# Kernel optimization log

Measured on AMD Instinct MI355X. Metric: run time of the kernel, lower is better.

## Reference

```python
import jax, jax.numpy as jnp
import numpy as np

H = W = 32
C = 512
RED = 16


def make_gus(v=1.5):
    # gus[p=(i,k), x, y] = exp(-((x-i)^2+(y-k)^2)/(2 v^2)) / (2 pi v^2), normalized per p.
    idx = np.arange(H, dtype=np.float64)
    d2 = (idx[:, None] - idx[None, :]) ** 2          # [center, coord]
    g1 = np.exp(-d2 / (2.0 * v * v))                  # separable factor
    g = np.einsum('ix,ky->ikxy', g1, g1) / (2.0 * np.pi * v * v)
    g = g / g.sum(axis=(2, 3), keepdims=True)         # per-position normalization
    return jnp.asarray(g.reshape(H * W, H, W), dtype=jnp.float32)


def setup_inputs() -> dict:
    key = jax.random.key(0)
    ks = jax.random.split(key, 6)
    b = 16
    return {
        'x': jax.random.normal(ks[0], (b, C, H, W), dtype=jnp.float32),
        'se_w1': jax.random.normal(ks[1], (C // RED, C), dtype=jnp.float32) * 0.02,
        'se_b1': jnp.zeros((C // RED,), dtype=jnp.float32),
        'se_w2': jax.random.normal(ks[2], (C, C // RED), dtype=jnp.float32) * 0.02,
        'se_b2': jnp.zeros((C,), dtype=jnp.float32),
        'down_w': jax.random.normal(ks[3], (C, 2 * C), dtype=jnp.float32) * 0.02,
        'gus': make_gus(1.5),
    }


def _patches3(img, h, w):
    # img: [b, c, h+2, w+2] -> [b, c, h, w, 9] (3x3 neighborhoods, row-major dy*3+dx)
    ps = [img[:, :, dy:dy + h, dx:dx + w] for dy in range(3) for dx in range(3)]
    return jnp.stack(ps, axis=-1)


def reference(x, se_w1, se_b1, se_w2, se_b2, down_w, gus):
    b, c, h, w = x.shape
    # --- SELayer ---
    s = x.mean(axis=(2, 3))                                   # [b, c]
    y = jax.nn.relu(s @ se_w1.T + se_b1)                       # [b, c/16]
    y = jax.nn.sigmoid(y @ se_w2.T + se_b2)                    # [b, c]
    out32 = x * y[:, :, None, None]
    # --- gaussian-weighted global pooling per output position ---
    # g[b, p, ch] = sum_{y,x} gus[p,y,x] * out32[b,ch,y,x]; then torch's view(c,h,w)
    gus_out = jnp.einsum('pyx,bcyx->bpc', gus, out32).reshape(b, c, h, w)
    # --- patch self-attention ---
    sig = jax.nn.sigmoid(out32)
    sigp = _patches3(jnp.pad(sig, ((0, 0), (0, 0), (1, 1), (1, 1))), h, w)    # [b,c,h,w,9]
    ffp = _patches3(jnp.pad(out32, ((0, 0), (0, 0), (1, 1), (1, 1))), h, w)   # [b,c,h,w,9]
    logits = jnp.einsum('bcyx,bcyxk->byxk', sig, sigp) / c     # mean over channels
    attn = jax.nn.softmax(logits, axis=-1)                     # softmax over 3x3 patch
    g2 = jnp.einsum('byxk,bcyxk->byxc', attn, ffp)             # [b,h,w,c] = [b, p, c]
    out_csa = g2.reshape(b, c, h, w)                           # torch view(c,h,w) of [hw,c]
    # --- down: 1x1 conv (no bias) + InstanceNorm2d + LeakyReLU(0.2) ---
    cat = jnp.concatenate([gus_out, out_csa], axis=1)          # [b, 2c, h, w]
    z = jnp.einsum('oi,biyx->boyx', down_w, cat)
    mu = z.mean(axis=(2, 3), keepdims=True)
    var = z.var(axis=(2, 3), keepdims=True)
    zn = (z - mu) * jax.lax.rsqrt(var + 1e-5)
    return jnp.where(zn >= 0, zn, 0.2 * zn)
```

## Files before the change

kernel.cpp:

```cpp
#include <hip/hip_runtime.h>
#include <stdint.h>

#define NB 16
#define NC 512
#define NS 1024
#define NR 32

typedef unsigned short u16;
typedef unsigned int u32;

typedef __attribute__((ext_vector_type(8))) short short8;
typedef __attribute__((ext_vector_type(4))) float f32x4;

__device__ __forceinline__ float bf2f(u16 u) {
    union { u32 i; float f; } c; c.i = ((u32)u) << 16; return c.f;
}
__device__ __forceinline__ u16 f2bf(float f) {
    union { float f; u32 i; } c; c.f = f;
    u32 r = (c.i + 0x7FFFu + ((c.i >> 16) & 1u)) >> 16;
    return (u16)r;
}
__device__ __forceinline__ float sigm(float x) {
    return 1.0f / (1.0f + __expf(-x));
}

__global__ void k_mean(const float* __restrict__ x, float* __restrict__ sm) {
    const int row = blockIdx.x;
    const float4* xr = (const float4*)(x + (long)row * NS);
    const int t = threadIdx.x;
    float4 v = xr[t];
    float p = v.x + v.y + v.z + v.w;
    for (int off = 32; off; off >>= 1) p += __shfl_down(p, off);
    __shared__ float red[4];
    if ((t & 63) == 0) red[t >> 6] = p;
    __syncthreads();
    if (t == 0) sm[row] = (red[0] + red[1] + red[2] + red[3]) * (1.0f / 1024.0f);
}

__global__ void k_se(const float* __restrict__ sm, const float* __restrict__ w1,
                     const float* __restrict__ b1, const float* __restrict__ w2,
                     const float* __restrict__ b2, float* __restrict__ y) {
    const int b = blockIdx.x;
    __shared__ float s_s[NC];
    __shared__ float s_y1[NR];
    const int t = threadIdx.x;
    s_s[t] = sm[b * NC + t];
    s_s[t + 256] = sm[b * NC + t + 256];
    __syncthreads();
    if (t < NR) {
        float acc = b1[t];
        for (int c = 0; c < NC; ++c) acc += s_s[c] * w1[t * NC + c];
        s_y1[t] = fmaxf(acc, 0.0f);
    }
    __syncthreads();
    for (int i = 0; i < 2; ++i) {
        int c = t + i * 256;
        float acc = b2[c];
#pragma unroll
        for (int r = 0; r < NR; ++r) acc += s_y1[r] * w2[c * NR + r];
        y[b * NC + c] = 1.0f / (1.0f + expf(-acc));
    }
}

__global__ void k_scale(const float* __restrict__ x, const float* __restrict__ y,
                        u16* __restrict__ o32, u16* __restrict__ o32t,
                        u16* __restrict__ sig_t) {
    const int b = blockIdx.z;
    const int c0 = blockIdx.y * 32;
    const int s0 = blockIdx.x * 32;
    const int tx = threadIdx.x & 31, ty = threadIdx.x >> 5;
    __shared__ float tile[32][33];
    const float* xb = x + (long)b * NC * NS;
#pragma unroll
    for (int it = 0; it < 4; ++it) {
        int c = c0 + ty + it * 8;
        float v = xb[(long)c * NS + s0 + tx] * y[b * NC + c];
        tile[ty + it * 8][tx] = v;
        o32[((long)b * NC + c) * NS + s0 + tx] = f2bf(v);
    }
    __syncthreads();
#pragma unroll
    for (int it = 0; it < 4; ++it) {
        int sr = ty + it * 8;
        float tv = tile[tx][sr];
        long idx = ((long)b * NS + (s0 + sr)) * NC + c0 + tx;
        o32t[idx] = f2bf(tv);
        sig_t[idx] = f2bf(sigm(tv));
    }
}

__global__ void k_cvt(const float* __restrict__ g, const float* __restrict__ dw,
                      u16* __restrict__ gb, u16* __restrict__ dwb) {
    const int i = blockIdx.x * 256 + threadIdx.x;
    gb[i] = f2bf(g[i]);
    if (i < 524288) dwb[i] = f2bf(dw[i]);
}

__device__ __forceinline__ void st_out(float* p, float v) { *p = v; }
__device__ __forceinline__ void st_out(u16* p, float v) { *p = f2bf(v); }

template <typename OT>
__global__ __launch_bounds__(256, 4)
void gemm_bt(const u16* __restrict__ A, const u16* __restrict__ Bt, OT* __restrict__ Co,
             int M, int N, int K, long batA, long batB, long batC) {
    const int b = blockIdx.z;
    const u16* Ab = A + (long)b * batA;
    const u16* Bb = Bt + (long)b * batB;
    OT* Cb = Co + (long)b * batC;
    const int m0 = blockIdx.y * 128, n0 = blockIdx.x * 64;
    __shared__ __align__(16) u16 As[128 * 64];
    __shared__ __align__(16) u16 Bs[64 * 64];
    const int tid = threadIdx.x;
    const int lane = tid & 63, wave = tid >> 6;
    const int wm = (wave >> 1) * 64, wn = (wave & 1) * 32;
    f32x4 acc[4][2];
#pragma unroll
    for (int i = 0; i < 4; ++i)
#pragma unroll
        for (int j = 0; j < 2; ++j) acc[i][j] = (f32x4){0.f, 0.f, 0.f, 0.f};

    const int erow = (tid * 8) >> 6;
    const int ecol = (tid * 8) & 63;

    for (int k0 = 0; k0 < K; k0 += 64) {
#pragma unroll
        for (int q = 0; q < 4; ++q) {
            const u16* ga = Ab + (long)(m0 + q * 32 + erow) * K + (k0 + ecol);
            __builtin_amdgcn_global_load_lds(
                (const __attribute__((address_space(1))) u32*)ga,
                (__attribute__((address_space(3))) u32*)&As[q * 2048 + tid * 8], 16, 0, 0);
        }
#pragma unroll
        for (int q = 0; q < 2; ++q) {
            const u16* gb = Bb + (long)(n0 + q * 32 + erow) * K + (k0 + ecol);
            __builtin_amdgcn_global_load_lds(
                (const __attribute__((address_space(1))) u32*)gb,
                (__attribute__((address_space(3))) u32*)&Bs[q * 2048 + tid * 8], 16, 0, 0);
        }
        __syncthreads();
#pragma unroll
        for (int kk = 0; kk < 64; kk += 32) {
            const int kidx = kk + ((lane >> 4) << 3);
            short8 af[4], bfr[2];
#pragma unroll
            for (int i = 0; i < 4; ++i)
                af[i] = *(const short8*)&As[(wm + i * 16 + (lane & 15)) * 64 + kidx];
#pragma unroll
            for (int j = 0; j < 2; ++j)
                bfr[j] = *(const short8*)&Bs[(wn + j * 16 + (lane & 15)) * 64 + kidx];
#pragma unroll
            for (int i = 0; i < 4; ++i)
#pragma unroll
                for (int j = 0; j < 2; ++j)
                    acc[i][j] = __builtin_amdgcn_mfma_f32_16x16x32_bf16(af[i], bfr[j], acc[i][j], 0, 0, 0);
        }
        __syncthreads();
    }
    const int col = lane & 15, rq = (lane >> 4) * 4;
#pragma unroll
    for (int i = 0; i < 4; ++i)
#pragma unroll
        for (int j = 0; j < 2; ++j)
#pragma unroll
            for (int r = 0; r < 4; ++r) {
                int row = m0 + wm + i * 16 + rq + r;
                int ncol = n0 + wn + j * 16 + col;
                st_out(&Cb[(long)row * N + ncol], acc[i][j][r]);
            }
}

__global__ __launch_bounds__(256)
void k_attn(const u16* __restrict__ sig_t, const u16* __restrict__ o32t,
            u16* __restrict__ g2) {
    const int wave = threadIdx.x >> 6, lane = threadIdx.x & 63;
    const int tid = threadIdx.x;
    const int bx = blockIdx.x;
    const int b = blockIdx.y;
    const int y0 = bx >> 3;
    const int xbase = (bx & 7) * 4;
    const long base = (long)b * NS * NC;
    __shared__ __align__(16) u16 smem[2 * 18 * NC];

#pragma unroll
    for (int r = 0; r < 9; ++r) {
        int idx = r * 256 + tid;
        int pair = idx >> 7;
        int rem = idx & 127;
        int arr = rem >> 6;
        int ch0 = (rem & 63) * 8;
        int yy = y0 + pair / 6 - 1;
        int xx = xbase + pair % 6 - 1;
        short8 v;
        if (yy >= 0 && yy < 32 && xx >= 0 && xx < 32) {
            long roff = base + (long)(yy * 32 + xx) * NC + ch0;
            v = arr ? *(const short8*)&o32t[roff] : *(const short8*)&sig_t[roff];
        } else {
            v = (short8){0, 0, 0, 0, 0, 0, 0, 0};
        }
        *(short8*)&smem[(arr * 18 + pair) * NC + ch0] = v;
    }
    __syncthreads();

    const int coff = lane * 8;
    short8 csv = *(const short8*)&smem[(6 + wave + 1) * NC + coff];
    float sc[8];
#pragma unroll
    for (int j = 0; j < 8; ++j) sc[j] = bf2f((u16)csv[j]);

    float part[9];
#pragma unroll
    for (int k = 0; k < 9; ++k) {
        int pair = (k / 3) * 6 + wave + k % 3;
        short8 sv = *(const short8*)&smem[pair * NC + coff];
        float p = 0.f;
#pragma unroll
        for (int j = 0; j < 8; ++j) p += sc[j] * bf2f((u16)sv[j]);
        part[k] = p;
    }
#pragma unroll
    for (int k = 0; k < 9; ++k)
        for (int off = 32; off; off >>= 1) part[k] += __shfl_down(part[k], off);

    if (lane == 0) {
        float mx = -1e30f;
#pragma unroll
        for (int k = 0; k < 9; ++k) { part[k] *= (1.0f / 512.0f); mx = fmaxf(mx, part[k]); }
        float sum = 0.f;
#pragma unroll
        for (int k = 0; k < 9; ++k) { part[k] = __expf(part[k] - mx); sum += part[k]; }
        float inv = 1.0f / sum;
#pragma unroll
        for (int k = 0; k < 9; ++k) part[k] *= inv;
    }
    float g[8] = {0.f, 0.f, 0.f, 0.f, 0.f, 0.f, 0.f, 0.f};
#pragma unroll
    for (int k = 0; k < 9; ++k) {
        float a = __shfl(part[k], 0);
        int pair = (k / 3) * 6 + wave + k % 3;
        short8 rv = *(const short8*)&smem[(18 + pair) * NC + coff];
#pragma unroll
        for (int j = 0; j < 8; ++j) g[j] += a * bf2f((u16)rv[j]);
    }
    short8 ov;
#pragma unroll
    for (int j = 0; j < 8; ++j) ov[j] = (short)f2bf(g[j]);
    const int s = y0 * 32 + xbase + wave;
    *(short8*)&g2[base + (long)s * NC + coff] = ov;
}

__global__ void k_tr(const u16* __restrict__ g, const u16* __restrict__ g2,
                     u16* __restrict__ ct) {
    const int b = blockIdx.z;
    const int i0 = blockIdx.y * 32, s0 = blockIdx.x * 32;
    const int tx = threadIdx.x & 31, ty = threadIdx.x >> 5;
    __shared__ u16 tile[32][33];
    const u16* src = (i0 < 512) ? (g + (long)b * 524288 + (long)i0 * 1024)
                                : (g2 + (long)b * 524288 + (long)(i0 - 512) * 1024);
#pragma unroll
    for (int it = 0; it < 4; ++it) {
        int il = ty + it * 8;
        tile[il][tx] = src[(long)il * 1024 + s0 + tx];
    }
    __syncthreads();
#pragma unroll
    for (int it = 0; it < 4; ++it) {
        int sl = ty + it * 8;
        ct[(long)b * 1048576 + (long)(s0 + sl) * 1024 + i0 + tx] = tile[tx][sl];
    }
}

__global__ void k_norm(const float* __restrict__ z, float* __restrict__ out) {
    const int row = blockIdx.x;
    const float4* zr = (const float4*)(z + (long)row * NS);
    const int t = threadIdx.x;
    float4 v = zr[t];
    float sm = v.x + v.y + v.z + v.w;
    float sq = v.x * v.x + v.y * v.y + v.z * v.z + v.w * v.w;
    for (int off = 32; off; off >>= 1) { sm += __shfl_down(sm, off); sq += __shfl_down(sq, off); }
    __shared__ float rs[4], rq2[4];
    if ((t & 63) == 0) { rs[t >> 6] = sm; rq2[t >> 6] = sq; }
    __syncthreads();
    float tot = rs[0] + rs[1] + rs[2] + rs[3];
    float totq = rq2[0] + rq2[1] + rq2[2] + rq2[3];
    float mu = tot * (1.0f / 1024.0f);
    float var = totq * (1.0f / 1024.0f) - mu * mu;
    float sc = rsqrtf(var + 1e-5f);
    float4 o;
    float a;
    a = (v.x - mu) * sc; o.x = (a >= 0.f) ? a : 0.2f * a;
    a = (v.y - mu) * sc; o.y = (a >= 0.f) ? a : 0.2f * a;
    a = (v.z - mu) * sc; o.z = (a >= 0.f) ? a : 0.2f * a;
    a = (v.w - mu) * sc; o.w = (a >= 0.f) ? a : 0.2f * a;
    ((float4*)(out + (long)row * NS))[t] = o;
}

extern "C" void kernel_launch(void* const* d_in, const int* in_sizes, int n_in,
                              void* d_out, int out_size, void* d_ws, size_t ws_size,
                              hipStream_t stream) {
    const float* x   = (const float*)d_in[0];
    const float* w1  = (const float*)d_in[1];
    const float* b1  = (const float*)d_in[2];
    const float* w2  = (const float*)d_in[3];
    const float* b2  = (const float*)d_in[4];
    const float* dw  = (const float*)d_in[5];
    const float* gus = (const float*)d_in[6];
    float* out = (float*)d_out;
    char* ws = (char*)d_ws;

    float* sm_buf = (float*)(ws + 0);
    float* y_buf  = (float*)(ws + 32768);
    u16* gusbf    = (u16*)(ws + 65536);
    u16* dwbf     = (u16*)(ws + 2162688);
    char* regA    = ws + 3211264;
    u16* o32      = (u16*)regA;
    u16* o32t     = (u16*)(regA + 16777216);
    u16* catT     = (u16*)regA;
    char* regB    = ws + 36765696;
    u16* sig_t    = (u16*)regB;
    u16* gbuf     = (u16*)regB;
    u16* g2b      = (u16*)(regB + 16777216);
    float* Z      = (float*)regB;

    k_mean<<<dim3(NB * NC), dim3(256), 0, stream>>>(x, sm_buf);
    k_se<<<dim3(NB), dim3(256), 0, stream>>>(sm_buf, w1, b1, w2, b2, y_buf);
    k_scale<<<dim3(32, 16, NB), dim3(256), 0, stream>>>(x, y_buf, o32, o32t, sig_t);
    k_cvt<<<dim3(4096), dim3(256), 0, stream>>>(gus, dw, gusbf, dwbf);
    k_attn<<<dim3(256, NB), dim3(256), 0, stream>>>(sig_t, o32t, g2b);
    gemm_bt<u16><<<dim3(8, 8, NB), dim3(256), 0, stream>>>(
        gusbf, o32, gbuf, 1024, 512, 1024, 0L, (long)NC * NS, (long)NC * NS);
    k_tr<<<dim3(32, 32, NB), dim3(256), 0, stream>>>(gbuf, g2b, catT);
    gemm_bt<float><<<dim3(16, 4, NB), dim3(256), 0, stream>>>(
        dwbf, catT, Z, 512, 1024, 1024, 0L, (long)NS * 1024, (long)NC * NS);
    k_norm<<<dim3(NB * NC), dim3(256), 0, stream>>>(Z, out);
}
```

Before: 231.9 us.

## Merge first GEMM with attention kernel, fuse mean with convert, use 128x128 GEMM tiles

Folds the bf16 conversion of gus and down_w into the channel-mean kernel as extra blocks. Runs the gaussian-pooling GEMM and the patch-attention kernel as one launch, with block index selecting the role and dynamic shared memory shared between them, so the two independent stages can overlap. Because the GEMM output can no longer alias sig_t, which attention is still reading, it moves to a separate workspace region. The shared GEMM body switches to 128x128 tiles with a 4x4 MFMA accumulator per wave. This raises register pressure, and the new buffer needs more workspace.

```diff
diff --git a/kernel.cpp b/kernel.cpp
--- a/kernel.cpp
+++ b/kernel.cpp
@@ -24,17 +24,25 @@
     return 1.0f / (1.0f + __expf(-x));
 }
 
-__global__ void k_mean(const float* __restrict__ x, float* __restrict__ sm) {
-    const int row = blockIdx.x;
-    const float4* xr = (const float4*)(x + (long)row * NS);
+__global__ void k_mean_cvt(const float* __restrict__ x, float* __restrict__ sm,
+                           const float* __restrict__ g, const float* __restrict__ dw,
+                           u16* __restrict__ gb, u16* __restrict__ dwb) {
     const int t = threadIdx.x;
-    float4 v = xr[t];
-    float p = v.x + v.y + v.z + v.w;
-    for (int off = 32; off; off >>= 1) p += __shfl_down(p, off);
-    __shared__ float red[4];
-    if ((t & 63) == 0) red[t >> 6] = p;
-    __syncthreads();
-    if (t == 0) sm[row] = (red[0] + red[1] + red[2] + red[3]) * (1.0f / 1024.0f);
+    if (blockIdx.x < NB * NC) {
+        const int row = blockIdx.x;
+        const float4* xr = (const float4*)(x + (long)row * NS);
+        float4 v = xr[t];
+        float p = v.x + v.y + v.z + v.w;
+        for (int off = 32; off; off >>= 1) p += __shfl_down(p, off);
+        __shared__ float red[4];
+        if ((t & 63) == 0) red[t >> 6] = p;
+        __syncthreads();
+        if (t == 0) sm[row] = (red[0] + red[1] + red[2] + red[3]) * (1.0f / 1024.0f);
+    } else {
+        const int i = (blockIdx.x - NB * NC) * 256 + t;
+        gb[i] = f2bf(g[i]);
+        if (i < 524288) dwb[i] = f2bf(dw[i]);
+    }
 }
 
 __global__ void k_se(const float* __restrict__ sm, const float* __restrict__ w1,
@@ -89,69 +97,58 @@
     }
 }
 
-__global__ void k_cvt(const float* __restrict__ g, const float* __restrict__ dw,
-                      u16* __restrict__ gb, u16* __restrict__ dwb) {
-    const int i = blockIdx.x * 256 + threadIdx.x;
-    gb[i] = f2bf(g[i]);
-    if (i < 524288) dwb[i] = f2bf(dw[i]);
-}
-
 __device__ __forceinline__ void st_out(float* p, float v) { *p = v; }
 __device__ __forceinline__ void st_out(u16* p, float v) { *p = f2bf(v); }
 
 template <typename OT>
-__global__ __launch_bounds__(256, 4)
-void gemm_bt(const u16* __restrict__ A, const u16* __restrict__ Bt, OT* __restrict__ Co,
-             int M, int N, int K, long batA, long batB, long batC) {
-    const int b = blockIdx.z;
-    const u16* Ab = A + (long)b * batA;
-    const u16* Bb = Bt + (long)b * batB;
-    OT* Cb = Co + (long)b * batC;
-    const int m0 = blockIdx.y * 128, n0 = blockIdx.x * 64;
-    __shared__ __align__(16) u16 As[128 * 64];
-    __shared__ __align__(16) u16 Bs[64 * 64];
+__device__ __forceinline__
+void gemm_body(const u16* __restrict__ Ab, const u16* __restrict__ Bb,
+               OT* __restrict__ Cb, int m0, int n0, int N, int K,
+               u16* As, u16* Bs) {
     const int tid = threadIdx.x;
     const int lane = tid & 63, wave = tid >> 6;
-    const int wm = (wave >> 1) * 64, wn = (wave & 1) * 32;
-    f32x4 acc[4][2];
+    const int wm = (wave >> 1) * 64, wn = (wave & 1) * 64;
+    f32x4 acc[4][4];
 #pragma unroll
     for (int i = 0; i < 4; ++i)
 #pragma unroll
-        for (int j = 0; j < 2; ++j) acc[i][j] = (f32x4){0.f, 0.f, 0.f, 0.f};
-
-    const int erow = (tid * 8) >> 6;
-    const int ecol = (tid * 8) & 63;
+        for (int j = 0; j < 4; ++j) acc[i][j] = (f32x4){0.f, 0.f, 0.f, 0.f};
+
+    int mrow[4], kcol[4];
+#pragma unroll
+    for (int q = 0; q < 4; ++q) {
+        int eoff = wave * 2048 + q * 512 + lane * 8;
+        mrow[q] = eoff >> 6;
+        kcol[q] = eoff & 63;
+    }
 
     for (int k0 = 0; k0 < K; k0 += 64) {
 #pragma unroll
         for (int q = 0; q < 4; ++q) {
-            const u16* ga = Ab + (long)(m0 + q * 32 + erow) * K + (k0 + ecol);
+            const u16* ga = Ab + (long)(m0 + mrow[q]) * K + (k0 + kcol[q]);
             __builtin_amdgcn_global_load_lds(
                 (const __attribute__((address_space(1))) u32*)ga,
-                (__attribute__((address_space(3))) u32*)&As[q * 2048 + tid * 8], 16, 0, 0);
-        }
-#pragma unroll
-        for (int q = 0; q < 2; ++q) {
-            const u16* gb = Bb + (long)(n0 + q * 32 + erow) * K + (k0 + ecol);
+                (__attribute__((address_space(3))) u32*)&As[wave * 2048 + q * 512], 16, 0, 0);
+            const u16* gb = Bb + (long)(n0 + mrow[q]) * K + (k0 + kcol[q]);
             __builtin_amdgcn_global_load_lds(
                 (const __attribute__((address_space(1))) u32*)gb,
-                (__attribute__((address_space(3))) u32*)&Bs[q * 2048 + tid * 8], 16, 0, 0);
+                (__attribute__((address_space(3))) u32*)&Bs[wave * 2048 + q * 512], 16, 0, 0);
         }
         __syncthreads();
 #pragma unroll
         for (int kk = 0; kk < 64; kk += 32) {
             const int kidx = kk + ((lane >> 4) << 3);
-            short8 af[4], bfr[2];
+            short8 af[4], bfr[4];
 #pragma unroll
             for (int i = 0; i < 4; ++i)
                 af[i] = *(const short8*)&As[(wm + i * 16 + (lane & 15)) * 64 + kidx];
 #pragma unroll
-            for (int j = 0; j < 2; ++j)
+            for (int j = 0; j < 4; ++j)
                 bfr[j] = *(const short8*)&Bs[(wn + j * 16 + (lane & 15)) * 64 + kidx];
 #pragma unroll
             for (int i = 0; i < 4; ++i)
 #pragma unroll
-                for (int j = 0; j < 2; ++j)
+                for (int j = 0; j < 4; ++j)
                     acc[i][j] = __builtin_amdgcn_mfma_f32_16x16x32_bf16(af[i], bfr[j], acc[i][j], 0, 0, 0);
         }
         __syncthreads();
@@ -160,7 +157,7 @@
 #pragma unroll
     for (int i = 0; i < 4; ++i)
 #pragma unroll
-        for (int j = 0; j < 2; ++j)
+        for (int j = 0; j < 4; ++j)
 #pragma unroll
             for (int r = 0; r < 4; ++r) {
                 int row = m0 + wm + i * 16 + rq + r;
@@ -170,16 +167,30 @@
 }
 
 __global__ __launch_bounds__(256)
-void k_attn(const u16* __restrict__ sig_t, const u16* __restrict__ o32t,
-            u16* __restrict__ g2) {
+void k_gemm1_attn(const u16* __restrict__ gusbf, const u16* __restrict__ o32,
+                  u16* __restrict__ gbuf, const u16* __restrict__ sig_t,
+                  const u16* __restrict__ o32t, u16* __restrict__ g2) {
+    extern __shared__ __align__(16) char dsm[];
+    if (blockIdx.x < 512) {
+        const int gx = blockIdx.x;
+        const int b = gx >> 5;
+        const int m0 = ((gx >> 2) & 7) * 128;
+        const int n0 = (gx & 3) * 128;
+        u16* As = (u16*)dsm;
+        u16* Bs = As + 128 * 64;
+        gemm_body<u16>(gusbf, o32 + (long)b * NC * NS, gbuf + (long)b * NC * NS,
+                       m0, n0, 512, 1024, As, Bs);
+        return;
+    }
+    const int id = blockIdx.x - 512;
+    const int bx = id & 255;
+    const int b = id >> 8;
     const int wave = threadIdx.x >> 6, lane = threadIdx.x & 63;
     const int tid = threadIdx.x;
-    const int bx = blockIdx.x;
-    const int b = blockIdx.y;
     const int y0 = bx >> 3;
     const int xbase = (bx & 7) * 4;
     const long base = (long)b * NS * NC;
-    __shared__ __align__(16) u16 smem[2 * 18 * NC];
+    u16* smem = (u16*)dsm;
 
 #pragma unroll
     for (int r = 0; r < 9; ++r) {
@@ -248,6 +259,17 @@
     *(short8*)&g2[base + (long)s * NC + coff] = ov;
 }
 
+template <typename OT>
+__global__ __launch_bounds__(256)
+void gemm_bt(const u16* __restrict__ A, const u16* __restrict__ Bt, OT* __restrict__ Co,
+             int M, int N, int K, long batA, long batB, long batC) {
+    const int b = blockIdx.z;
+    __shared__ __align__(16) u16 As[128 * 64];
+    __shared__ __align__(16) u16 Bs[128 * 64];
+    gemm_body<OT>(A + (long)b * batA, Bt + (long)b * batB, Co + (long)b * batC,
+                  blockIdx.y * 128, blockIdx.x * 128, N, K, As, Bs);
+}
+
 __global__ void k_tr(const u16* __restrict__ g, const u16* __restrict__ g2,
                      u16* __restrict__ ct) {
     const int b = blockIdx.z;
@@ -321,15 +343,16 @@
     u16* g2b      = (u16*)(regB + 16777216);
     float* Z      = (float*)regB;
 
-    k_mean<<<dim3(NB * NC), dim3(256), 0, stream>>>(x, sm_buf);
+    u16* gbuf_safe = (u16*)(ws + 3211264 + 33554432);
+    (void)gbuf; (void)gbuf_safe;
+    u16* gbuf2 = (u16*)(ws + 36765696 + 33554432);
+
+    k_mean_cvt<<<dim3(NB * NC + 4096), dim3(256), 0, stream>>>(x, sm_buf, gus, dw, gusbf, dwbf);
     k_se<<<dim3(NB), dim3(256), 0, stream>>>(sm_buf, w1, b1, w2, b2, y_buf);
     k_scale<<<dim3(32, 16, NB), dim3(256), 0, stream>>>(x, y_buf, o32, o32t, sig_t);
-    k_cvt<<<dim3(4096), dim3(256), 0, stream>>>(gus, dw, gusbf, dwbf);
-    k_attn<<<dim3(256, NB), dim3(256), 0, stream>>>(sig_t, o32t, g2b);
-    gemm_bt<u16><<<dim3(8, 8, NB), dim3(256), 0, stream>>>(
-        gusbf, o32, gbuf, 1024, 512, 1024, 0L, (long)NC * NS, (long)NC * NS);
-    k_tr<<<dim3(32, 32, NB), dim3(256), 0, stream>>>(gbuf, g2b, catT);
-    gemm_bt<float><<<dim3(16, 4, NB), dim3(256), 0, stream>>>(
+    k_gemm1_attn<<<dim3(4608), dim3(256), 36864, stream>>>(gusbf, o32, gbuf2, sig_t, o32t, g2b);
+    k_tr<<<dim3(32, 32, NB), dim3(256), 0, stream>>>(gbuf2, g2b, catT);
+    gemm_bt<float><<<dim3(8, 4, NB), dim3(256), 0, stream>>>(
         dwbf, catT, Z, 512, 1024, 1024, 0L, (long)NS * 1024, (long)NC * NS);
     k_norm<<<dim3(NB * NC), dim3(256), 0, stream>>>(Z, out);
 }
```

After: 236.5 us. Within noise of the previous version (+2.0%).

## Enlarge GEMM tile to 128x128 with XOR-swizzled LDS and fuse conversion kernel

Applied to the files above, without the earlier changes.

The batched bf16 GEMM tile grows from 128x64 to 128x128, so each wave computes a 64x64 sub-tile with 16 MFMA accumulators. This raises arithmetic intensity per LDS load and halves the grid size. LDS staging now uses an XOR swizzle on 16-byte groups to avoid bank conflicts on the fragment reads. The separate gus/down_w bf16 conversion kernel is folded into the channel-mean kernel as extra blocks, saving one launch. The larger tile uses more registers and drops the occupancy hint in launch_bounds.

```diff
diff --git a/kernel.cpp b/kernel.cpp
--- a/kernel.cpp
+++ b/kernel.cpp
@@ -24,17 +24,25 @@
     return 1.0f / (1.0f + __expf(-x));
 }
 
-__global__ void k_mean(const float* __restrict__ x, float* __restrict__ sm) {
-    const int row = blockIdx.x;
-    const float4* xr = (const float4*)(x + (long)row * NS);
+__global__ void k_mean_cvt(const float* __restrict__ x, float* __restrict__ sm,
+                           const float* __restrict__ g, const float* __restrict__ dw,
+                           u16* __restrict__ gb, u16* __restrict__ dwb) {
     const int t = threadIdx.x;
-    float4 v = xr[t];
-    float p = v.x + v.y + v.z + v.w;
-    for (int off = 32; off; off >>= 1) p += __shfl_down(p, off);
-    __shared__ float red[4];
-    if ((t & 63) == 0) red[t >> 6] = p;
-    __syncthreads();
-    if (t == 0) sm[row] = (red[0] + red[1] + red[2] + red[3]) * (1.0f / 1024.0f);
+    if (blockIdx.x < NB * NC) {
+        const int row = blockIdx.x;
+        const float4* xr = (const float4*)(x + (long)row * NS);
+        float4 v = xr[t];
+        float p = v.x + v.y + v.z + v.w;
+        for (int off = 32; off; off >>= 1) p += __shfl_down(p, off);
+        __shared__ float red[4];
+        if ((t & 63) == 0) red[t >> 6] = p;
+        __syncthreads();
+        if (t == 0) sm[row] = (red[0] + red[1] + red[2] + red[3]) * (1.0f / 1024.0f);
+    } else {
+        const int i = (blockIdx.x - NB * NC) * 256 + t;
+        gb[i] = f2bf(g[i]);
+        if (i < 524288) dwb[i] = f2bf(dw[i]);
+    }
 }
 
 __global__ void k_se(const float* __restrict__ sm, const float* __restrict__ w1,
@@ -89,69 +97,62 @@
     }
 }
 
-__global__ void k_cvt(const float* __restrict__ g, const float* __restrict__ dw,
-                      u16* __restrict__ gb, u16* __restrict__ dwb) {
-    const int i = blockIdx.x * 256 + threadIdx.x;
-    gb[i] = f2bf(g[i]);
-    if (i < 524288) dwb[i] = f2bf(dw[i]);
-}
-
 __device__ __forceinline__ void st_out(float* p, float v) { *p = v; }
 __device__ __forceinline__ void st_out(u16* p, float v) { *p = f2bf(v); }
 
 template <typename OT>
-__global__ __launch_bounds__(256, 4)
+__global__ __launch_bounds__(256)
 void gemm_bt(const u16* __restrict__ A, const u16* __restrict__ Bt, OT* __restrict__ Co,
              int M, int N, int K, long batA, long batB, long batC) {
     const int b = blockIdx.z;
     const u16* Ab = A + (long)b * batA;
     const u16* Bb = Bt + (long)b * batB;
     OT* Cb = Co + (long)b * batC;
-    const int m0 = blockIdx.y * 128, n0 = blockIdx.x * 64;
+    const int m0 = blockIdx.y * 128, n0 = blockIdx.x * 128;
     __shared__ __align__(16) u16 As[128 * 64];
-    __shared__ __align__(16) u16 Bs[64 * 64];
+    __shared__ __align__(16) u16 Bs[128 * 64];
     const int tid = threadIdx.x;
     const int lane = tid & 63, wave = tid >> 6;
-    const int wm = (wave >> 1) * 64, wn = (wave & 1) * 32;
-    f32x4 acc[4][2];
+    const int wm = (wave >> 1) * 64, wn = (wave & 1) * 64;
+    f32x4 acc[4][4];
 #pragma unroll
     for (int i = 0; i < 4; ++i)
 #pragma unroll
-        for (int j = 0; j < 2; ++j) acc[i][j] = (f32x4){0.f, 0.f, 0.f, 0.f};
-
-    const int erow = (tid * 8) >> 6;
-    const int ecol = (tid * 8) & 63;
+        for (int j = 0; j < 4; ++j) acc[i][j] = (f32x4){0.f, 0.f, 0.f, 0.f};
+
+    const int srow = lane >> 3;
+    const int sgr = (lane & 7) ^ srow;
+    const int ldsoff = lane * 8;
 
     for (int k0 = 0; k0 < K; k0 += 64) {
 #pragma unroll
         for (int q = 0; q < 4; ++q) {
-            const u16* ga = Ab + (long)(m0 + q * 32 + erow) * K + (k0 + ecol);
+            const int rl = wave * 32 + q * 8 + srow;
+            const u16* ga = Ab + (long)(m0 + rl) * K + (k0 + sgr * 8);
             __builtin_amdgcn_global_load_lds(
                 (const __attribute__((address_space(1))) u32*)ga,
-                (__attribute__((address_space(3))) u32*)&As[q * 2048 + tid * 8], 16, 0, 0);
-        }
-#pragma unroll
-        for (int q = 0; q < 2; ++q) {
-            const u16* gb = Bb + (long)(n0 + q * 32 + erow) * K + (k0 + ecol);
+                (__attribute__((address_space(3))) u32*)&As[wave * 2048 + q * 512 + ldsoff], 16, 0, 0);
+            const u16* gb = Bb + (long)(n0 + rl) * K + (k0 + sgr * 8);
             __builtin_amdgcn_global_load_lds(
                 (const __attribute__((address_space(1))) u32*)gb,
-                (__attribute__((address_space(3))) u32*)&Bs[q * 2048 + tid * 8], 16, 0, 0);
+                (__attribute__((address_space(3))) u32*)&Bs[wave * 2048 + q * 512 + ldsoff], 16, 0, 0);
         }
         __syncthreads();
 #pragma unroll
         for (int kk = 0; kk < 64; kk += 32) {
-            const int kidx = kk + ((lane >> 4) << 3);
-            short8 af[4], bfr[2];
+            const int gq = (kk >> 3) + (lane >> 4);
+            const int slot = gq ^ (lane & 7);
+            short8 af[4], bfr[4];
 #pragma unroll
             for (int i = 0; i < 4; ++i)
-                af[i] = *(const short8*)&As[(wm + i * 16 + (lane & 15)) * 64 + kidx];
-#pragma unroll
-            for (int j = 0; j < 2; ++j)
-                bfr[j] = *(const short8*)&Bs[(wn + j * 16 + (lane & 15)) * 64 + kidx];
+                af[i] = *(const short8*)&As[(wm + i * 16 + (lane & 15)) * 64 + slot * 8];
+#pragma unroll
+            for (int j = 0; j < 4; ++j)
+                bfr[j] = *(const short8*)&Bs[(wn + j * 16 + (lane & 15)) * 64 + slot * 8];
 #pragma unroll
             for (int i = 0; i < 4; ++i)
 #pragma unroll
-                for (int j = 0; j < 2; ++j)
+                for (int j = 0; j < 4; ++j)
                     acc[i][j] = __builtin_amdgcn_mfma_f32_16x16x32_bf16(af[i], bfr[j], acc[i][j], 0, 0, 0);
         }
         __syncthreads();
@@ -160,7 +161,7 @@
 #pragma unroll
     for (int i = 0; i < 4; ++i)
 #pragma unroll
-        for (int j = 0; j < 2; ++j)
+        for (int j = 0; j < 4; ++j)
 #pragma unroll
             for (int r = 0; r < 4; ++r) {
                 int row = m0 + wm + i * 16 + rq + r;
@@ -321,15 +322,14 @@
     u16* g2b      = (u16*)(regB + 16777216);
     float* Z      = (float*)regB;
 
-    k_mean<<<dim3(NB * NC), dim3(256), 0, stream>>>(x, sm_buf);
+    k_mean_cvt<<<dim3(NB * NC + 4096), dim3(256), 0, stream>>>(x, sm_buf, gus, dw, gusbf, dwbf);
     k_se<<<dim3(NB), dim3(256), 0, stream>>>(sm_buf, w1, b1, w2, b2, y_buf);
     k_scale<<<dim3(32, 16, NB), dim3(256), 0, stream>>>(x, y_buf, o32, o32t, sig_t);
-    k_cvt<<<dim3(4096), dim3(256), 0, stream>>>(gus, dw, gusbf, dwbf);
     k_attn<<<dim3(256, NB), dim3(256), 0, stream>>>(sig_t, o32t, g2b);
-    gemm_bt<u16><<<dim3(8, 8, NB), dim3(256), 0, stream>>>(
+    gemm_bt<u16><<<dim3(4, 8, NB), dim3(256), 0, stream>>>(
         gusbf, o32, gbuf, 1024, 512, 1024, 0L, (long)NC * NS, (long)NC * NS);
     k_tr<<<dim3(32, 32, NB), dim3(256), 0, stream>>>(gbuf, g2b, catT);
-    gemm_bt<float><<<dim3(16, 4, NB), dim3(256), 0, stream>>>(
+    gemm_bt<float><<<dim3(8, 4, NB), dim3(256), 0, stream>>>(
         dwbf, catT, Z, 512, 1024, 1024, 0L, (long)NS * 1024, (long)NC * NS);
     k_norm<<<dim3(NB * NC), dim3(256), 0, stream>>>(Z, out);
 }
```

Measured after the change: 220.9 us. 1.05x faster.
